# Kernel tuning notes

Hardware: AMD Instinct MI355X
Metric: run time of the kernel (lower is better)

## Reference

```python
import jax, jax.numpy as jnp
import numpy as np

B, T, D = 4, 8192, 512
N_LEVELS = 3
N_HEAD = 4
HEAD_DIM = D // N_HEAD
STRIDES = (8, 4, 4)
SEGS = (T // 8, T // 32, T // 128)  # 1024, 256, 64 segments per level
LN_EPS = 1e-5


def setup_inputs() -> dict:
    key = jax.random.key(0)
    ks = jax.random.split(key, 8)
    h_bytes = jax.random.normal(ks[0], (B, T, D), jnp.float32)
    def strided_boundaries(length, stride):
        b = np.zeros((B, length), np.int32)
        b[:, ::stride] = 1  # segment-start markers; first position always a boundary
        return jnp.asarray(b)
    b0 = strided_boundaries(T, STRIDES[0])
    b1 = strided_boundaries(SEGS[0], STRIDES[1])
    b2 = strided_boundaries(SEGS[1], STRIDES[2])
    s = 0.02
    return dict(
        h_bytes=h_bytes, b0=b0, b1=b1, b2=b2,
        mlp_ln_g=jnp.ones((N_LEVELS, D), jnp.float32),
        mlp_ln_b=jnp.zeros((N_LEVELS, D), jnp.float32),
        mlp_w1=jax.random.normal(ks[1], (N_LEVELS, D, 2 * D), jnp.float32) * s,
        mlp_b1=jnp.zeros((N_LEVELS, 2 * D), jnp.float32),
        mlp_w2=jax.random.normal(ks[2], (N_LEVELS, 2 * D, D), jnp.float32) * s,
        mlp_b2=jnp.zeros((N_LEVELS, D), jnp.float32),
        # 8 linears per cross-level block: bu_q,bu_k,bu_v,bu_out,td_q,td_k,td_v,td_out
        ca_w=jax.random.normal(ks[3], (N_LEVELS - 1, 8, D, D), jnp.float32) * s,
        ca_b=jnp.zeros((N_LEVELS - 1, 8, D), jnp.float32),
        ca_ln_g=jnp.ones((N_LEVELS - 1, 2, D), jnp.float32),  # [.,0]=bu_norm, [.,1]=td_norm
        ca_ln_b=jnp.zeros((N_LEVELS - 1, 2, D), jnp.float32),
    )


def _ln(x, g, b):
    mu = jnp.mean(x, axis=-1, keepdims=True)
    xc = x - mu
    var = jnp.mean(xc * xc, axis=-1, keepdims=True)
    return xc * jax.lax.rsqrt(var + LN_EPS) * g + b


def _mha(xq, xkv, Wq, Wk, Wv, Wo, bq, bk, bv, bo):
    Bq, Sq, _ = xq.shape
    Skv = xkv.shape[1]
    q = (xq @ Wq + bq).reshape(Bq, Sq, N_HEAD, HEAD_DIM)
    k = (xkv @ Wk + bk).reshape(Bq, Skv, N_HEAD, HEAD_DIM)
    v = (xkv @ Wv + bv).reshape(Bq, Skv, N_HEAD, HEAD_DIM)
    scores = jnp.einsum('bqhd,bkhd->bhqk', q, k) * (1.0 / (HEAD_DIM ** 0.5))
    att = jax.nn.softmax(scores, axis=-1)
    out = jnp.einsum('bhqk,bkhd->bqhd', att, v).reshape(Bq, Sq, D)
    return out @ Wo + bo


def _segment_mean_pool(x, seg_ids, n_seg):
    # x: [B, T, D], seg_ids: [B, T] in [0, n_seg)
    sums = jax.vmap(lambda xi, si: jax.ops.segment_sum(xi, si, num_segments=n_seg))(x, seg_ids)
    cnts = jax.vmap(lambda si: jax.ops.segment_sum(jnp.ones(si.shape, jnp.float32), si, num_segments=n_seg))(seg_ids)
    return sums / jnp.maximum(cnts, 1.0)[..., None]


def reference(h_bytes, b0, b1, b2, mlp_ln_g, mlp_ln_b, mlp_w1, mlp_b1, mlp_w2, mlp_b2, ca_w, ca_b, ca_ln_g, ca_ln_b):
    bounds = (b0, b1, b2)
    segs = []
    cur = h_bytes
    for lvl in range(N_LEVELS):
        seg_ids = jnp.cumsum(bounds[lvl], axis=1) - 1  # boundary marks segment start
        pooled = _segment_mean_pool(cur, seg_ids, SEGS[lvl])
        h = _ln(pooled, mlp_ln_g[lvl], mlp_ln_b[lvl])
        h = jax.nn.gelu(h @ mlp_w1[lvl] + mlp_b1[lvl], approximate=False)
        pooled = pooled + (h @ mlp_w2[lvl] + mlp_b2[lvl])
        segs.append(pooled)
        cur = pooled
    # top-down cross-level refinement
    for i in range(N_LEVELS - 2, -1, -1):
        fine, coarse = segs[i], segs[i + 1]
        fn = _ln(fine, ca_ln_g[i, 0], ca_ln_b[i, 0])
        fu = fine + _mha(fn, coarse, ca_w[i, 0], ca_w[i, 1], ca_w[i, 2], ca_w[i, 3],
                         ca_b[i, 0], ca_b[i, 1], ca_b[i, 2], ca_b[i, 3])
        cn = _ln(coarse, ca_ln_g[i, 1], ca_ln_b[i, 1])
        cu = coarse + _mha(cn, fu, ca_w[i, 4], ca_w[i, 5], ca_w[i, 6], ca_w[i, 7],
                           ca_b[i, 4], ca_b[i, 5], ca_b[i, 6], ca_b[i, 7])
        segs[i], segs[i + 1] = fu, cu
    return tuple(segs)
```

## Files before the change

kernel.cpp:

```cpp
#include <hip/hip_runtime.h>
#include <hip/hip_bf16.h>
#include <math.h>

typedef __attribute__((ext_vector_type(8))) short bf16x8;
typedef __attribute__((ext_vector_type(4))) float f32x4;
typedef unsigned short u16;

__device__ __forceinline__ u16 f2b(float f) {
  unsigned u = __float_as_uint(f);
  u = u + 0x7fffu + ((u >> 16) & 1u);
  return (u16)(u >> 16);
}
__device__ __forceinline__ float gelu_exact(float x) {
  return 0.5f * x * (1.0f + erff(x * 0.70710678118654752f));
}

__global__ __launch_bounds__(1024) void scan_all_k(
    const int* __restrict__ b0, const int* __restrict__ b1,
    const int* __restrict__ b2, int* __restrict__ starts) {
  __shared__ int sums[1024];
  int lvl = blockIdx.y, row = blockIdx.x;
  const int* bp = (lvl == 0) ? b0 : (lvl == 1) ? b1 : b2;
  int n = (lvl == 0) ? 8192 : (lvl == 1) ? 1024 : 256;
  int nseg = (lvl == 0) ? 1024 : (lvl == 1) ? 256 : 64;
  int* sp = starts + ((lvl == 0) ? 0 : (lvl == 1) ? 4096 : 5120);
  const int* br = bp + (size_t)row * n;
  int chunk = (n + 1023) / 1024;
  int t0 = threadIdx.x * chunk;
  int t1 = t0 + chunk; if (t1 > n) t1 = n;
  if (t0 > n) t0 = n;
  int s = 0;
  for (int t = t0; t < t1; ++t) s += br[t];
  sums[threadIdx.x] = s;
  __syncthreads();
  for (int off = 1; off < 1024; off <<= 1) {
    int v = (threadIdx.x >= off) ? sums[threadIdx.x - off] : 0;
    __syncthreads();
    sums[threadIdx.x] += v;
    __syncthreads();
  }
  int run = sums[threadIdx.x] - s;
  for (int t = t0; t < t1; ++t) {
    if (br[t]) { sp[(size_t)row * nseg + run] = t; ++run; }
  }
}

__global__ __launch_bounds__(256) void wtrans_all_k(
    const float* __restrict__ w1, const float* __restrict__ w2,
    const float* __restrict__ ca, u16* __restrict__ w1t,
    u16* __restrict__ w2t, u16* __restrict__ cat) {
  __shared__ float tile[32][33];
  int z = blockIdx.x;
  const float* W; u16* Wt; int K, M, m0, k0;
  if (z < 1536) {
    int mat = z >> 9, tl = z & 511;
    W = w1 + (size_t)mat * 524288; Wt = w1t + (size_t)mat * 524288;
    K = 512; M = 1024; m0 = (tl & 31) * 32; k0 = (tl >> 5) * 32;
  } else if (z < 3072) {
    z -= 1536; int mat = z >> 9, tl = z & 511;
    W = w2 + (size_t)mat * 524288; Wt = w2t + (size_t)mat * 524288;
    K = 1024; M = 512; m0 = (tl & 15) * 32; k0 = (tl >> 4) * 32;
  } else {
    z -= 3072; int mat = z >> 8, tl = z & 255;
    W = ca + (size_t)mat * 262144; Wt = cat + (size_t)mat * 262144;
    K = 512; M = 512; m0 = (tl & 15) * 32; k0 = (tl >> 4) * 32;
  }
  int x = threadIdx.x & 31, y = threadIdx.x >> 5;
  #pragma unroll
  for (int i = 0; i < 32; i += 8)
    tile[y + i][x] = W[(size_t)(k0 + y + i) * M + m0 + x];
  __syncthreads();
  #pragma unroll
  for (int i = 0; i < 32; i += 8)
    Wt[(size_t)(m0 + y + i) * K + k0 + x] = f2b(tile[x][y + i]);
}

__global__ __launch_bounds__(256) void pool_ln_k(
    const float* __restrict__ x, const int* __restrict__ starts,
    float* __restrict__ pooled, const float* __restrict__ g,
    const float* __restrict__ bt, u16* __restrict__ lnout,
    int Tin, int nseg) {
  int wv = threadIdx.x >> 6, lane = threadIdx.x & 63;
  int s = blockIdx.x * 4 + wv, b = blockIdx.y;
  int st = starts[(size_t)b * nseg + s];
  int en = (s + 1 < nseg) ? starts[(size_t)b * nseg + s + 1] : Tin;
  const float* xb = x + ((size_t)b * Tin) * 512;
  int d = lane * 8;
  float a[8] = {0.f,0.f,0.f,0.f,0.f,0.f,0.f,0.f};
  for (int t = st; t < en; ++t) {
    const float* row = xb + (size_t)t * 512 + d;
    float4 v0 = *(const float4*)row;
    float4 v1 = *(const float4*)(row + 4);
    a[0]+=v0.x; a[1]+=v0.y; a[2]+=v0.z; a[3]+=v0.w;
    a[4]+=v1.x; a[5]+=v1.y; a[6]+=v1.z; a[7]+=v1.w;
  }
  int cnt = en - st; if (cnt < 1) cnt = 1;
  float ic = 1.0f / (float)cnt;
  #pragma unroll
  for (int i = 0; i < 8; ++i) a[i] *= ic;
  int tok = b * nseg + s;
  float* pr = pooled + (size_t)tok * 512 + d;
  *(float4*)pr = make_float4(a[0], a[1], a[2], a[3]);
  *(float4*)(pr + 4) = make_float4(a[4], a[5], a[6], a[7]);
  float sm = a[0]+a[1]+a[2]+a[3]+a[4]+a[5]+a[6]+a[7];
  #pragma unroll
  for (int off = 32; off; off >>= 1) sm += __shfl_xor(sm, off, 64);
  float mean = sm * (1.0f / 512.0f);
  float ss = 0.f;
  #pragma unroll
  for (int i = 0; i < 8; ++i) { a[i] -= mean; ss += a[i]*a[i]; }
  #pragma unroll
  for (int off = 32; off; off >>= 1) ss += __shfl_xor(ss, off, 64);
  float inv = rsqrtf(ss * (1.0f / 512.0f) + 1e-5f);
  float4 g0 = *(const float4*)(g + d), g1 = *(const float4*)(g + d + 4);
  float4 b0 = *(const float4*)(bt + d), b1 = *(const float4*)(bt + d + 4);
  float gg[8] = {g0.x,g0.y,g0.z,g0.w,g1.x,g1.y,g1.z,g1.w};
  float bb[8] = {b0.x,b0.y,b0.z,b0.w,b1.x,b1.y,b1.z,b1.w};
  union { u16 u[8]; uint4 v; } pk;
  #pragma unroll
  for (int i = 0; i < 8; ++i) pk.u[i] = f2b(a[i] * inv * gg[i] + bb[i]);
  *(uint4*)(lnout + (size_t)tok * 512 + d) = pk.v;
}

__global__ __launch_bounds__(256) void ln_kernel(
    const float* __restrict__ x, const float* __restrict__ g,
    const float* __restrict__ bt, u16* __restrict__ y, int ntok) {
  int wave = threadIdx.x >> 6, lane = threadIdx.x & 63;
  int tok = blockIdx.x * 4 + wave;
  if (tok >= ntok) return;
  const float* xr = x + (size_t)tok * 512;
  int d = lane * 8;
  float4 v0 = *(const float4*)(xr + d);
  float4 v1 = *(const float4*)(xr + d + 4);
  float s = v0.x + v0.y + v0.z + v0.w + v1.x + v1.y + v1.z + v1.w;
  #pragma unroll
  for (int off = 32; off; off >>= 1) s += __shfl_xor(s, off, 64);
  float mean = s * (1.0f / 512.0f);
  float a[8] = {v0.x-mean, v0.y-mean, v0.z-mean, v0.w-mean,
                v1.x-mean, v1.y-mean, v1.z-mean, v1.w-mean};
  float ss = 0.f;
  #pragma unroll
  for (int i = 0; i < 8; ++i) ss += a[i]*a[i];
  #pragma unroll
  for (int off = 32; off; off >>= 1) ss += __shfl_xor(ss, off, 64);
  float inv = rsqrtf(ss * (1.0f / 512.0f) + 1e-5f);
  float4 g0 = *(const float4*)(g + d), g1 = *(const float4*)(g + d + 4);
  float4 b0 = *(const float4*)(bt + d), b1 = *(const float4*)(bt + d + 4);
  float gg[8] = {g0.x,g0.y,g0.z,g0.w,g1.x,g1.y,g1.z,g1.w};
  float bb[8] = {b0.x,b0.y,b0.z,b0.w,b1.x,b1.y,b1.z,b1.w};
  union { u16 u[8]; uint4 v; } pk;
  #pragma unroll
  for (int i = 0; i < 8; ++i) pk.u[i] = f2b(a[i] * inv * gg[i] + bb[i]);
  *(uint4*)(y + (size_t)tok * 512 + d) = pk.v;
}

__global__ __launch_bounds__(256) void vtrans_kernel(
    const u16* __restrict__ vsrc, int lds_, u16* __restrict__ vT, int Skv) {
  __shared__ u16 tile[32][33];
  int kv0 = blockIdx.x * 32, d0 = blockIdx.y * 32;
  int z = blockIdx.z, b = z >> 2, h = z & 3;
  const u16* src = vsrc + ((size_t)b * Skv) * lds_ + h * 128;
  u16* dst = vT + (size_t)z * 128 * Skv;
  int x = threadIdx.x & 31, y = threadIdx.x >> 5;
  #pragma unroll
  for (int i = 0; i < 32; i += 8)
    tile[y + i][x] = src[(size_t)(kv0 + y + i) * lds_ + d0 + x];
  __syncthreads();
  #pragma unroll
  for (int i = 0; i < 32; i += 8)
    dst[(size_t)(d0 + y + i) * Skv + kv0 + x] = tile[x][y + i];
}

__device__ __forceinline__ void mfma_core(
    const u16* __restrict__ A, int lda, const u16* __restrict__ Wt, int ldw,
    int K, u16* AsB, u16* WsB, f32x4 acc[2][2]) {
  int t = threadIdx.x;
  int lane = t & 63, wave = t >> 6;
  int wr = (wave >> 1) * 32, wc = (wave & 1) * 32;
  int lrow = t >> 3;
  int lseg = t & 7;
  int swz = (lseg * 16) ^ ((lrow & 7) << 4);
  const u16* Ap0 = A + (size_t)lrow * lda + lseg * 8;
  const u16* Ap1 = Ap0 + (size_t)32 * lda;
  const u16* Wp0 = Wt + (size_t)lrow * ldw + lseg * 8;
  const u16* Wp1 = Wp0 + (size_t)32 * ldw;
  uint4 a0 = *(const uint4*)(Ap0);
  uint4 a1 = *(const uint4*)(Ap1);
  uint4 w0 = *(const uint4*)(Wp0);
  uint4 w1 = *(const uint4*)(Wp1);
  for (int k0 = 0; k0 < K; k0 += 64) {
    __syncthreads();
    *(uint4*)((char*)AsB + lrow * 128 + swz) = a0;
    *(uint4*)((char*)AsB + (lrow + 32) * 128 + swz) = a1;
    *(uint4*)((char*)WsB + lrow * 128 + swz) = w0;
    *(uint4*)((char*)WsB + (lrow + 32) * 128 + swz) = w1;
    __syncthreads();
    if (k0 + 64 < K) {
      a0 = *(const uint4*)(Ap0 + k0 + 64);
      a1 = *(const uint4*)(Ap1 + k0 + 64);
      w0 = *(const uint4*)(Wp0 + k0 + 64);
      w1 = *(const uint4*)(Wp1 + k0 + 64);
    }
    #pragma unroll
    for (int ks = 0; ks < 2; ++ks) {
      bf16x8 af[2], bfr[2];
      #pragma unroll
      for (int mi = 0; mi < 2; ++mi) {
        int row = wr + mi * 16 + (lane & 15);
        int cb = (ks * 64 + ((lane >> 4) << 4)) ^ ((row & 7) << 4);
        af[mi] = *(const bf16x8*)((const char*)AsB + row * 128 + cb);
      }
      #pragma unroll
      for (int ni = 0; ni < 2; ++ni) {
        int row = wc + ni * 16 + (lane & 15);
        int cb = (ks * 64 + ((lane >> 4) << 4)) ^ ((row & 7) << 4);
        bfr[ni] = *(const bf16x8*)((const char*)WsB + row * 128 + cb);
      }
      #pragma unroll
      for (int mi = 0; mi < 2; ++mi)
        #pragma unroll
        for (int ni = 0; ni < 2; ++ni)
          acc[mi][ni] = __builtin_amdgcn_mfma_f32_16x16x32_bf16(
              af[mi], bfr[ni], acc[mi][ni], 0, 0, 0);
    }
  }
}

__global__ __launch_bounds__(256) void gemm_k(
    const u16* __restrict__ A, int lda, const u16* __restrict__ Wt, int ldw,
    int K, const float* __restrict__ bias, float* __restrict__ Cf,
    u16* __restrict__ Cb, int ldc, int flags) {
  __shared__ u16 As[4096], Ws[4096];
  int n0 = blockIdx.y * 64, m0 = blockIdx.x * 64;
  f32x4 acc[2][2];
  #pragma unroll
  for (int i = 0; i < 2; ++i)
    #pragma unroll
    for (int j = 0; j < 2; ++j) acc[i][j] = (f32x4){0.f, 0.f, 0.f, 0.f};
  mfma_core(A + (size_t)n0 * lda, lda, Wt + (size_t)m0 * ldw, ldw, K, As, Ws, acc);
  int lane = threadIdx.x & 63, wave = threadIdx.x >> 6;
  int wr = (wave >> 1) * 32, wc = (wave & 1) * 32;
  #pragma unroll
  for (int mi = 0; mi < 2; ++mi) {
    #pragma unroll
    for (int ni = 0; ni < 2; ++ni) {
      int col = m0 + wc + ni * 16 + (lane & 15);
      float bv = bias[col];
      #pragma unroll
      for (int j = 0; j < 4; ++j) {
        int row = n0 + wr + mi * 16 + ((lane >> 4) << 2) + j;
        float v = acc[mi][ni][j] + bv;
        if (flags & 1) v = gelu_exact(v);
        size_t idx = (size_t)row * ldc + col;
        if (flags & 2) v += Cf[idx];
        if (flags & 4) Cf[idx] = v;
        if (flags & 8) Cb[idx] = f2b(v);
      }
    }
  }
}

__global__ __launch_bounds__(256) void fattn_k(
    const u16* __restrict__ Q, int ldq, const u16* __restrict__ KV, int ldkv,
    const u16* __restrict__ vT, u16* __restrict__ O, int ldo,
    int Sq, int Skv) {
  __shared__ u16 Ps[4][16 * 64];
  __shared__ float Ob[3][8][16][16];
  __shared__ float Ls[3][16];
  int z = blockIdx.y, b = z >> 2, h = z & 3;
  int t = threadIdx.x, lane = t & 63, w = t >> 6;
  int g = lane >> 4, ql = lane & 15;
  int q0 = blockIdx.x * 16;
  const float scale = 0.08838834764831845f;
  bf16x8 qf[4];
  {
    const u16* qp = Q + ((size_t)(b * Sq + q0 + ql)) * ldq + h * 128 + g * 8;
    #pragma unroll
    for (int ks = 0; ks < 4; ++ks) qf[ks] = *(const bf16x8*)(qp + 32 * ks);
  }
  f32x4 o[8];
  #pragma unroll
  for (int i = 0; i < 8; ++i) o[i] = (f32x4){0.f, 0.f, 0.f, 0.f};
  float lsum = 0.f;
  int ntiles = Skv >> 6;
  const u16* kbaseA = KV + ((size_t)b * Skv + ql) * ldkv + h * 128 + g * 8;
  const u16* vbase = vT + (size_t)z * 128 * Skv;
  for (int tt = w; tt < ntiles; tt += 4) {
    int kv0 = tt * 64;
    float rs = 0.f;
    #pragma unroll
    for (int kvt = 0; kvt < 4; ++kvt) {
      const u16* kp = kbaseA + (size_t)(kv0 + kvt * 16) * ldkv;
      f32x4 acc = (f32x4){0.f, 0.f, 0.f, 0.f};
      #pragma unroll
      for (int ks = 0; ks < 4; ++ks) {
        bf16x8 kf = *(const bf16x8*)(kp + 32 * ks);
        acc = __builtin_amdgcn_mfma_f32_16x16x32_bf16(kf, qf[ks], acc, 0, 0, 0);
      }
      float e0 = __expf(acc[0] * scale), e1 = __expf(acc[1] * scale);
      float e2 = __expf(acc[2] * scale), e3 = __expf(acc[3] * scale);
      rs += e0 + e1 + e2 + e3;
      unsigned lo = (unsigned)f2b(e0) | ((unsigned)f2b(e1) << 16);
      unsigned hi = (unsigned)f2b(e2) | ((unsigned)f2b(e3) << 16);
      int slot = (2 * kvt + (g >> 1)) ^ (ql & 7);
      *(uint2*)((char*)Ps[w] + ql * 128 + slot * 16 + 8 * (g & 1)) =
          make_uint2(lo, hi);
    }
    rs += __shfl_xor(rs, 16, 64);
    rs += __shfl_xor(rs, 32, 64);
    lsum += rs;
    #pragma unroll
    for (int kh = 0; kh < 2; ++kh) {
      int slot = (4 * kh + g) ^ (ql & 7);
      bf16x8 pa = *(const bf16x8*)((const char*)Ps[w] + ql * 128 + slot * 16);
      #pragma unroll
      for (int dt = 0; dt < 8; ++dt) {
        bf16x8 vf = *(const bf16x8*)(vbase + (size_t)(dt * 16 + ql) * Skv +
                                     kv0 + kh * 32 + g * 8);
        o[dt] = __builtin_amdgcn_mfma_f32_16x16x32_bf16(pa, vf, o[dt], 0, 0, 0);
      }
    }
  }
  if (w) {
    #pragma unroll
    for (int dt = 0; dt < 8; ++dt)
      #pragma unroll
      for (int j = 0; j < 4; ++j)
        Ob[w - 1][dt][4 * g + j][ql] = o[dt][j];
    if (g == 0) Ls[w - 1][ql] = lsum;
  }
  __syncthreads();
  if (w == 0) {
    float lt = lsum + Ls[0][ql] + Ls[1][ql] + Ls[2][ql];
    float linv[4];
    #pragma unroll
    for (int r = 0; r < 4; ++r) linv[r] = 1.0f / __shfl(lt, 4 * g + r, 64);
    u16* ob = O + ((size_t)(b * Sq + q0)) * ldo + h * 128;
    #pragma unroll
    for (int dt = 0; dt < 8; ++dt)
      #pragma unroll
      for (int r = 0; r < 4; ++r) {
        float v = o[dt][r] + Ob[0][dt][4 * g + r][ql] +
                  Ob[1][dt][4 * g + r][ql] + Ob[2][dt][4 * g + r][ql];
        ob[(size_t)(4 * g + r) * ldo + dt * 16 + ql] = f2b(v * linv[r]);
      }
  }
}

extern "C" void kernel_launch(void* const* d_in, const int* in_sizes, int n_in,
                              void* d_out, int out_size, void* d_ws, size_t ws_size,
                              hipStream_t stream) {
  (void)in_sizes; (void)n_in; (void)out_size; (void)ws_size;
  const float* h_bytes  = (const float*)d_in[0];
  const int*   b0       = (const int*)d_in[1];
  const int*   b1       = (const int*)d_in[2];
  const int*   b2       = (const int*)d_in[3];
  const float* mlp_ln_g = (const float*)d_in[4];
  const float* mlp_ln_b = (const float*)d_in[5];
  const float* mlp_w1   = (const float*)d_in[6];
  const float* mlp_b1   = (const float*)d_in[7];
  const float* mlp_w2   = (const float*)d_in[8];
  const float* mlp_b2   = (const float*)d_in[9];
  const float* ca_w     = (const float*)d_in[10];
  const float* ca_b     = (const float*)d_in[11];
  const float* ca_ln_g  = (const float*)d_in[12];
  const float* ca_ln_b  = (const float*)d_in[13];

  float* out0 = (float*)d_out;
  float* out1 = out0 + 4 * 1024 * 512;
  float* out2 = out1 + 4 * 256 * 512;

  char* wsb = (char*)d_ws;
  const size_t MB = 1048576;
  u16* w1t   = (u16*)(wsb + 0 * MB);
  u16* w2t   = (u16*)(wsb + 3 * MB);
  u16* cat   = (u16*)(wsb + 6 * MB);
  u16* m0b   = (u16*)(wsb + 14 * MB);
  u16* m1b   = (u16*)(wsb + 18 * MB);
  u16* m2b   = (u16*)(wsb + 19 * MB);
  u16* lnbuf = (u16*)(wsb + 20 * MB);
  u16* hbuf  = (u16*)(wsb + 24 * MB);
  u16* qb    = (u16*)(wsb + 32 * MB);
  u16* kvbuf = (u16*)(wsb + 36 * MB);
  u16* vT    = (u16*)(wsb + 44 * MB);
  u16* abuf  = (u16*)(wsb + 48 * MB);
  int* starts  = (int*)(wsb + 52 * MB);
  int* starts0 = starts;
  int* starts1 = starts + 4096;
  int* starts2 = starts + 5120;

  wtrans_all_k<<<7168, 256, 0, stream>>>(mlp_w1, mlp_w2, ca_w, w1t, w2t, cat);
  scan_all_k<<<dim3(4, 3), 1024, 0, stream>>>(b0, b1, b2, starts);

  auto mlp = [&](float* X, u16* mir, int Ntok, int lvl) {
    gemm_k<<<dim3(16, Ntok / 64), 256, 0, stream>>>(
        lnbuf, 512, w1t + (size_t)lvl * 524288, 512, 512,
        mlp_b1 + lvl * 1024, nullptr, hbuf, 1024, 1 | 8);
    gemm_k<<<dim3(8, Ntok / 64), 256, 0, stream>>>(
        hbuf, 1024, w2t + (size_t)lvl * 524288, 1024, 1024,
        mlp_b2 + lvl * 512, X, mir, 512, 2 | 4 | 8);
  };
  pool_ln_k<<<dim3(256, 4), 256, 0, stream>>>(h_bytes, starts0, out0,
      mlp_ln_g, mlp_ln_b, lnbuf, 8192, 1024);
  mlp(out0, m0b, 4096, 0);
  pool_ln_k<<<dim3(64, 4), 256, 0, stream>>>(out0, starts1, out1,
      mlp_ln_g + 512, mlp_ln_b + 512, lnbuf, 1024, 256);
  mlp(out1, m1b, 1024, 1);
  pool_ln_k<<<dim3(16, 4), 256, 0, stream>>>(out1, starts2, out2,
      mlp_ln_g + 1024, mlp_ln_b + 1024, lnbuf, 256, 64);
  mlp(out2, m2b, 256, 2);

  auto cross = [&](int i, float* F, u16* mf, float* Cc, u16* mc, int nf, int nc) {
    u16* cw = cat + (size_t)i * 8 * 262144;
    const float* bb = ca_b + (size_t)i * 8 * 512;
    const float* lg = ca_ln_g + (size_t)i * 2 * 512;
    const float* lb = ca_ln_b + (size_t)i * 2 * 512;
    int Nf = 4 * nf, Nc = 4 * nc;
    ln_kernel<<<Nf / 4, 256, 0, stream>>>(F, lg, lb, lnbuf, Nf);
    gemm_k<<<dim3(8, Nf / 64), 256, 0, stream>>>(lnbuf, 512, cw, 512, 512,
        bb, nullptr, qb, 512, 8);
    gemm_k<<<dim3(16, Nc / 64), 256, 0, stream>>>(mc, 512, cw + 262144, 512, 512,
        bb + 512, nullptr, kvbuf, 1024, 8);
    vtrans_kernel<<<dim3(nc / 32, 4, 16), 256, 0, stream>>>(kvbuf + 512, 1024, vT, nc);
    fattn_k<<<dim3(nf / 16, 16), 256, 0, stream>>>(qb, 512, kvbuf, 1024, vT,
        abuf, 512, nf, nc);
    gemm_k<<<dim3(8, Nf / 64), 256, 0, stream>>>(abuf, 512, cw + 3 * 262144, 512, 512,
        bb + 3 * 512, F, mf, 512, 2 | 4 | 8);
    ln_kernel<<<Nc / 4, 256, 0, stream>>>(Cc, lg + 512, lb + 512, lnbuf, Nc);
    gemm_k<<<dim3(8, Nc / 64), 256, 0, stream>>>(lnbuf, 512, cw + 4 * 262144, 512, 512,
        bb + 4 * 512, nullptr, qb, 512, 8);
    gemm_k<<<dim3(16, Nf / 64), 256, 0, stream>>>(mf, 512, cw + 5 * 262144, 512, 512,
        bb + 5 * 512, nullptr, kvbuf, 1024, 8);
    vtrans_kernel<<<dim3(nf / 32, 4, 16), 256, 0, stream>>>(kvbuf + 512, 1024, vT, nf);
    fattn_k<<<dim3(nc / 16, 16), 256, 0, stream>>>(qb, 512, kvbuf, 1024, vT,
        abuf, 512, nc, nf);
    gemm_k<<<dim3(8, Nc / 64), 256, 0, stream>>>(abuf, 512, cw + 7 * 262144, 512, 512,
        bb + 7 * 512, Cc, mc, 512, 2 | 4 | 8);
  };
  cross(1, out1, m1b, out2, m2b, 256, 64);
  cross(0, out0, m0b, out1, m1b, 1024, 256);
}
```

Measured before the change: 443.0 us.

## Fuse LN, GEMM and V-transpose into multi-job kernels to cut launches

Merges the weight transpose and boundary scan into one kernel and replaces the separate LayerNorm, GEMM and V-transpose launches with a single fused kernel that dispatches LN blocks and up to two GEMM jobs by block index. The K/V projection writes V already transposed through a shared-memory tile, which removes the vtrans pass. Independent stages, such as the next LayerNorm alongside the output projection and the Q and KV GEMMs, now run in one grid. Bf16 mirror writes that are never read are dropped. This reduces launch count and serialization, at the cost of more branching and a larger shared-memory footprint per block.

```diff
diff --git a/kernel.cpp b/kernel.cpp
--- a/kernel.cpp
+++ b/kernel.cpp
@@ -15,42 +15,47 @@
   return 0.5f * x * (1.0f + erff(x * 0.70710678118654752f));
 }
 
-__global__ __launch_bounds__(1024) void scan_all_k(
+struct GemmJob {
+  const u16* A; const u16* Wt; const float* bias;
+  float* Cf; u16* Cb; u16* vT;
+  int lda, ldw, K, ldc, flags, bx, nblk, Skv;
+};
+struct LnJob { const float* x; const float* g; const float* b; u16* y; int ntok, nblk; };
+
+__global__ __launch_bounds__(256) void wtrans_scan_k(
+    const float* __restrict__ w1, const float* __restrict__ w2,
+    const float* __restrict__ ca, u16* __restrict__ w1t,
+    u16* __restrict__ w2t, u16* __restrict__ cat,
     const int* __restrict__ b0, const int* __restrict__ b1,
     const int* __restrict__ b2, int* __restrict__ starts) {
-  __shared__ int sums[1024];
-  int lvl = blockIdx.y, row = blockIdx.x;
-  const int* bp = (lvl == 0) ? b0 : (lvl == 1) ? b1 : b2;
-  int n = (lvl == 0) ? 8192 : (lvl == 1) ? 1024 : 256;
-  int nseg = (lvl == 0) ? 1024 : (lvl == 1) ? 256 : 64;
-  int* sp = starts + ((lvl == 0) ? 0 : (lvl == 1) ? 4096 : 5120);
-  const int* br = bp + (size_t)row * n;
-  int chunk = (n + 1023) / 1024;
-  int t0 = threadIdx.x * chunk;
-  int t1 = t0 + chunk; if (t1 > n) t1 = n;
-  if (t0 > n) t0 = n;
-  int s = 0;
-  for (int t = t0; t < t1; ++t) s += br[t];
-  sums[threadIdx.x] = s;
-  __syncthreads();
-  for (int off = 1; off < 1024; off <<= 1) {
-    int v = (threadIdx.x >= off) ? sums[threadIdx.x - off] : 0;
+  __shared__ char smbuf[32 * 33 * 4];
+  int z = blockIdx.x;
+  if (z >= 7168) {
+    int* sums = (int*)smbuf;
+    int j = z - 7168, lvl = j >> 2, row = j & 3;
+    const int* bp = (lvl == 0) ? b0 : (lvl == 1) ? b1 : b2;
+    int n = (lvl == 0) ? 8192 : (lvl == 1) ? 1024 : 256;
+    int nseg = (lvl == 0) ? 1024 : (lvl == 1) ? 256 : 64;
+    int* sp = starts + ((lvl == 0) ? 0 : (lvl == 1) ? 4096 : 5120);
+    const int* br = bp + (size_t)row * n;
+    int chunk = n >> 8;
+    int t0 = threadIdx.x * chunk, t1 = t0 + chunk;
+    int s = 0;
+    for (int t = t0; t < t1; ++t) s += br[t];
+    sums[threadIdx.x] = s;
     __syncthreads();
-    sums[threadIdx.x] += v;
-    __syncthreads();
-  }
-  int run = sums[threadIdx.x] - s;
-  for (int t = t0; t < t1; ++t) {
-    if (br[t]) { sp[(size_t)row * nseg + run] = t; ++run; }
-  }
-}
-
-__global__ __launch_bounds__(256) void wtrans_all_k(
-    const float* __restrict__ w1, const float* __restrict__ w2,
-    const float* __restrict__ ca, u16* __restrict__ w1t,
-    u16* __restrict__ w2t, u16* __restrict__ cat) {
-  __shared__ float tile[32][33];
-  int z = blockIdx.x;
+    for (int off = 1; off < 256; off <<= 1) {
+      int v = (threadIdx.x >= off) ? sums[threadIdx.x - off] : 0;
+      __syncthreads();
+      sums[threadIdx.x] += v;
+      __syncthreads();
+    }
+    int run = sums[threadIdx.x] - s;
+    for (int t = t0; t < t1; ++t)
+      if (br[t]) { sp[(size_t)row * nseg + run] = t; ++run; }
+    return;
+  }
+  float (*tile)[33] = (float(*)[33])smbuf;
   const float* W; u16* Wt; int K, M, m0, k0;
   if (z < 1536) {
     int mat = z >> 9, tl = z & 511;
@@ -120,55 +125,6 @@
   #pragma unroll
   for (int i = 0; i < 8; ++i) pk.u[i] = f2b(a[i] * inv * gg[i] + bb[i]);
   *(uint4*)(lnout + (size_t)tok * 512 + d) = pk.v;
-}
-
-__global__ __launch_bounds__(256) void ln_kernel(
-    const float* __restrict__ x, const float* __restrict__ g,
-    const float* __restrict__ bt, u16* __restrict__ y, int ntok) {
-  int wave = threadIdx.x >> 6, lane = threadIdx.x & 63;
-  int tok = blockIdx.x * 4 + wave;
-  if (tok >= ntok) return;
-  const float* xr = x + (size_t)tok * 512;
-  int d = lane * 8;
-  float4 v0 = *(const float4*)(xr + d);
-  float4 v1 = *(const float4*)(xr + d + 4);
-  float s = v0.x + v0.y + v0.z + v0.w + v1.x + v1.y + v1.z + v1.w;
-  #pragma unroll
-  for (int off = 32; off; off >>= 1) s += __shfl_xor(s, off, 64);
-  float mean = s * (1.0f / 512.0f);
-  float a[8] = {v0.x-mean, v0.y-mean, v0.z-mean, v0.w-mean,
-                v1.x-mean, v1.y-mean, v1.z-mean, v1.w-mean};
-  float ss = 0.f;
-  #pragma unroll
-  for (int i = 0; i < 8; ++i) ss += a[i]*a[i];
-  #pragma unroll
-  for (int off = 32; off; off >>= 1) ss += __shfl_xor(ss, off, 64);
-  float inv = rsqrtf(ss * (1.0f / 512.0f) + 1e-5f);
-  float4 g0 = *(const float4*)(g + d), g1 = *(const float4*)(g + d + 4);
-  float4 b0 = *(const float4*)(bt + d), b1 = *(const float4*)(bt + d + 4);
-  float gg[8] = {g0.x,g0.y,g0.z,g0.w,g1.x,g1.y,g1.z,g1.w};
-  float bb[8] = {b0.x,b0.y,b0.z,b0.w,b1.x,b1.y,b1.z,b1.w};
-  union { u16 u[8]; uint4 v; } pk;
-  #pragma unroll
-  for (int i = 0; i < 8; ++i) pk.u[i] = f2b(a[i] * inv * gg[i] + bb[i]);
-  *(uint4*)(y + (size_t)tok * 512 + d) = pk.v;
-}
-
-__global__ __launch_bounds__(256) void vtrans_kernel(
-    const u16* __restrict__ vsrc, int lds_, u16* __restrict__ vT, int Skv) {
-  __shared__ u16 tile[32][33];
-  int kv0 = blockIdx.x * 32, d0 = blockIdx.y * 32;
-  int z = blockIdx.z, b = z >> 2, h = z & 3;
-  const u16* src = vsrc + ((size_t)b * Skv) * lds_ + h * 128;
-  u16* dst = vT + (size_t)z * 128 * Skv;
-  int x = threadIdx.x & 31, y = threadIdx.x >> 5;
-  #pragma unroll
-  for (int i = 0; i < 32; i += 8)
-    tile[y + i][x] = src[(size_t)(kv0 + y + i) * lds_ + d0 + x];
-  __syncthreads();
-  #pragma unroll
-  for (int i = 0; i < 32; i += 8)
-    dst[(size_t)(d0 + y + i) * Skv + kv0 + x] = tile[x][y + i];
 }
 
 __device__ __forceinline__ void mfma_core(
@@ -226,37 +182,108 @@
   }
 }
 
-__global__ __launch_bounds__(256) void gemm_k(
-    const u16* __restrict__ A, int lda, const u16* __restrict__ Wt, int ldw,
-    int K, const float* __restrict__ bias, float* __restrict__ Cf,
-    u16* __restrict__ Cb, int ldc, int flags) {
-  __shared__ u16 As[4096], Ws[4096];
-  int n0 = blockIdx.y * 64, m0 = blockIdx.x * 64;
+__device__ __forceinline__ void gemm_body(const GemmJob& J, int mx, int my,
+                                          char* smem) {
+  u16* As = (u16*)smem;
+  u16* Ws = As + 4096;
+  int n0 = my * 64, m0 = mx * 64;
   f32x4 acc[2][2];
   #pragma unroll
   for (int i = 0; i < 2; ++i)
     #pragma unroll
     for (int j = 0; j < 2; ++j) acc[i][j] = (f32x4){0.f, 0.f, 0.f, 0.f};
-  mfma_core(A + (size_t)n0 * lda, lda, Wt + (size_t)m0 * ldw, ldw, K, As, Ws, acc);
+  mfma_core(J.A + (size_t)n0 * J.lda, J.lda, J.Wt + (size_t)m0 * J.ldw, J.ldw,
+            J.K, As, Ws, acc);
   int lane = threadIdx.x & 63, wave = threadIdx.x >> 6;
   int wr = (wave >> 1) * 32, wc = (wave & 1) * 32;
+  if ((J.flags & 16) && m0 >= 512) {
+    __syncthreads();
+    u16* tile = (u16*)smem;
+    #pragma unroll
+    for (int mi = 0; mi < 2; ++mi)
+      #pragma unroll
+      for (int ni = 0; ni < 2; ++ni) {
+        int tc = wc + ni * 16 + (lane & 15);
+        float bv = J.bias[m0 + tc];
+        #pragma unroll
+        for (int j = 0; j < 4; ++j) {
+          int tr = wr + mi * 16 + ((lane >> 4) << 2) + j;
+          tile[tr * 72 + tc] = f2b(acc[mi][ni][j] + bv);
+        }
+      }
+    __syncthreads();
+    int h = (m0 - 512) >> 7, d0i = (m0 - 512) & 127;
+    int b = n0 / J.Skv, tok0 = n0 % J.Skv;
+    int z = b * 4 + h;
+    int d = threadIdx.x >> 2, tkb = (threadIdx.x & 3) * 16;
+    u16* dst = J.vT + ((size_t)z * 128 + d0i + d) * J.Skv + tok0 + tkb;
+    union { u16 u[16]; uint4 v[2]; } pk;
+    #pragma unroll
+    for (int t2 = 0; t2 < 16; ++t2) pk.u[t2] = tile[(tkb + t2) * 72 + d];
+    *(uint4*)dst = pk.v[0];
+    *(uint4*)(dst + 8) = pk.v[1];
+    return;
+  }
   #pragma unroll
   for (int mi = 0; mi < 2; ++mi) {
     #pragma unroll
     for (int ni = 0; ni < 2; ++ni) {
       int col = m0 + wc + ni * 16 + (lane & 15);
-      float bv = bias[col];
+      float bv = J.bias[col];
       #pragma unroll
       for (int j = 0; j < 4; ++j) {
         int row = n0 + wr + mi * 16 + ((lane >> 4) << 2) + j;
         float v = acc[mi][ni][j] + bv;
-        if (flags & 1) v = gelu_exact(v);
-        size_t idx = (size_t)row * ldc + col;
-        if (flags & 2) v += Cf[idx];
-        if (flags & 4) Cf[idx] = v;
-        if (flags & 8) Cb[idx] = f2b(v);
+        if (J.flags & 1) v = gelu_exact(v);
+        size_t idx = (size_t)row * J.ldc + col;
+        if (J.flags & 2) v += J.Cf[idx];
+        if (J.flags & 4) J.Cf[idx] = v;
+        if (J.flags & 8) J.Cb[idx] = f2b(v);
       }
     }
+  }
+}
+
+__device__ __forceinline__ void ln_body(const LnJob& L, int bid) {
+  int wave = threadIdx.x >> 6, lane = threadIdx.x & 63;
+  int tok = bid * 4 + wave;
+  if (tok >= L.ntok) return;
+  const float* xr = L.x + (size_t)tok * 512;
+  int d = lane * 8;
+  float4 v0 = *(const float4*)(xr + d);
+  float4 v1 = *(const float4*)(xr + d + 4);
+  float s = v0.x + v0.y + v0.z + v0.w + v1.x + v1.y + v1.z + v1.w;
+  #pragma unroll
+  for (int off = 32; off; off >>= 1) s += __shfl_xor(s, off, 64);
+  float mean = s * (1.0f / 512.0f);
+  float a[8] = {v0.x-mean, v0.y-mean, v0.z-mean, v0.w-mean,
+                v1.x-mean, v1.y-mean, v1.z-mean, v1.w-mean};
+  float ss = 0.f;
+  #pragma unroll
+  for (int i = 0; i < 8; ++i) ss += a[i]*a[i];
+  #pragma unroll
+  for (int off = 32; off; off >>= 1) ss += __shfl_xor(ss, off, 64);
+  float inv = rsqrtf(ss * (1.0f / 512.0f) + 1e-5f);
+  float4 g0 = *(const float4*)(L.g + d), g1 = *(const float4*)(L.g + d + 4);
+  float4 b0 = *(const float4*)(L.b + d), b1 = *(const float4*)(L.b + d + 4);
+  float gg[8] = {g0.x,g0.y,g0.z,g0.w,g1.x,g1.y,g1.z,g1.w};
+  float bb[8] = {b0.x,b0.y,b0.z,b0.w,b1.x,b1.y,b1.z,b1.w};
+  union { u16 u[8]; uint4 v; } pk;
+  #pragma unroll
+  for (int i = 0; i < 8; ++i) pk.u[i] = f2b(a[i] * inv * gg[i] + bb[i]);
+  *(uint4*)(L.y + (size_t)tok * 512 + d) = pk.v;
+}
+
+__global__ __launch_bounds__(256) void fused_k(LnJob L, GemmJob A, GemmJob B) {
+  __shared__ char smem[16384];
+  int bid = blockIdx.x;
+  if (bid < L.nblk) { ln_body(L, bid); return; }
+  bid -= L.nblk;
+  if (bid < A.nblk) {
+    gemm_body(A, bid % A.bx, bid / A.bx, smem);
+  } else {
+    bid -= A.nblk;
+    gemm_body(B, bid % B.bx, bid / B.bx, smem);
   }
 }
 
@@ -381,7 +408,7 @@
   u16* lnbuf = (u16*)(wsb + 20 * MB);
   u16* hbuf  = (u16*)(wsb + 24 * MB);
   u16* qb    = (u16*)(wsb + 32 * MB);
-  u16* kvbuf = (u16*)(wsb + 36 * MB);
+  u16* kbuf  = (u16*)(wsb + 36 * MB);
   u16* vT    = (u16*)(wsb + 44 * MB);
   u16* abuf  = (u16*)(wsb + 48 * MB);
   int* starts  = (int*)(wsb + 52 * MB);
@@ -389,54 +416,90 @@
   int* starts1 = starts + 4096;
   int* starts2 = starts + 5120;
 
-  wtrans_all_k<<<7168, 256, 0, stream>>>(mlp_w1, mlp_w2, ca_w, w1t, w2t, cat);
-  scan_all_k<<<dim3(4, 3), 1024, 0, stream>>>(b0, b1, b2, starts);
-
-  auto mlp = [&](float* X, u16* mir, int Ntok, int lvl) {
-    gemm_k<<<dim3(16, Ntok / 64), 256, 0, stream>>>(
-        lnbuf, 512, w1t + (size_t)lvl * 524288, 512, 512,
-        mlp_b1 + lvl * 1024, nullptr, hbuf, 1024, 1 | 8);
-    gemm_k<<<dim3(8, Ntok / 64), 256, 0, stream>>>(
-        hbuf, 1024, w2t + (size_t)lvl * 524288, 1024, 1024,
-        mlp_b2 + lvl * 512, X, mir, 512, 2 | 4 | 8);
+  auto mkgemm = [](const u16* A, int lda, const u16* Wt, int ldw, int K,
+                   const float* bias, float* Cf, u16* Cb, int ldc, int flags,
+                   int rows, int M, u16* vTp = nullptr, int Skv = 0) {
+    GemmJob j; j.A = A; j.lda = lda; j.Wt = Wt; j.ldw = ldw; j.K = K;
+    j.bias = bias; j.Cf = Cf; j.Cb = Cb; j.ldc = ldc; j.flags = flags;
+    j.bx = M / 64; j.nblk = (M / 64) * (rows / 64); j.vT = vTp; j.Skv = Skv;
+    return j;
   };
+  auto mkln = [](const float* x, const float* g, const float* b, u16* y,
+                 int ntok) {
+    LnJob l; l.x = x; l.g = g; l.b = b; l.y = y; l.ntok = ntok;
+    l.nblk = ntok / 4; return l;
+  };
+  GemmJob gz = {}; gz.nblk = 0; gz.bx = 1;
+  LnJob lz = {}; lz.nblk = 0;
+  auto launch = [&](LnJob L, GemmJob A, GemmJob B) {
+    fused_k<<<L.nblk + A.nblk + B.nblk, 256, 0, stream>>>(L, A, B);
+  };
+
+  wtrans_scan_k<<<7180, 256, 0, stream>>>(mlp_w1, mlp_w2, ca_w, w1t, w2t, cat,
+                                          b0, b1, b2, starts);
+
   pool_ln_k<<<dim3(256, 4), 256, 0, stream>>>(h_bytes, starts0, out0,
       mlp_ln_g, mlp_ln_b, lnbuf, 8192, 1024);
-  mlp(out0, m0b, 4096, 0);
+  launch(lz, mkgemm(lnbuf, 512, w1t, 512, 512, mlp_b1, nullptr, hbuf, 1024,
+                    1 | 8, 4096, 1024), gz);
+  launch(lz, mkgemm(hbuf, 1024, w2t, 1024, 1024, mlp_b2, out0, nullptr, 512,
+                    2 | 4, 4096, 512), gz);
   pool_ln_k<<<dim3(64, 4), 256, 0, stream>>>(out0, starts1, out1,
       mlp_ln_g + 512, mlp_ln_b + 512, lnbuf, 1024, 256);
-  mlp(out1, m1b, 1024, 1);
+  launch(lz, mkgemm(lnbuf, 512, w1t + 524288, 512, 512, mlp_b1 + 1024,
+                    nullptr, hbuf, 1024, 1 | 8, 1024, 1024), gz);
+  launch(lz, mkgemm(hbuf, 1024, w2t + 524288, 1024, 1024, mlp_b2 + 512, out1,
+                    nullptr, 512, 2 | 4, 1024, 512), gz);
   pool_ln_k<<<dim3(16, 4), 256, 0, stream>>>(out1, starts2, out2,
       mlp_ln_g + 1024, mlp_ln_b + 1024, lnbuf, 256, 64);
-  mlp(out2, m2b, 256, 2);
-
-  auto cross = [&](int i, float* F, u16* mf, float* Cc, u16* mc, int nf, int nc) {
-    u16* cw = cat + (size_t)i * 8 * 262144;
-    const float* bb = ca_b + (size_t)i * 8 * 512;
-    const float* lg = ca_ln_g + (size_t)i * 2 * 512;
-    const float* lb = ca_ln_b + (size_t)i * 2 * 512;
-    int Nf = 4 * nf, Nc = 4 * nc;
-    ln_kernel<<<Nf / 4, 256, 0, stream>>>(F, lg, lb, lnbuf, Nf);
-    gemm_k<<<dim3(8, Nf / 64), 256, 0, stream>>>(lnbuf, 512, cw, 512, 512,
-        bb, nullptr, qb, 512, 8);
-    gemm_k<<<dim3(16, Nc / 64), 256, 0, stream>>>(mc, 512, cw + 262144, 512, 512,
-        bb + 512, nullptr, kvbuf, 1024, 8);
-    vtrans_kernel<<<dim3(nc / 32, 4, 16), 256, 0, stream>>>(kvbuf + 512, 1024, vT, nc);
-    fattn_k<<<dim3(nf / 16, 16), 256, 0, stream>>>(qb, 512, kvbuf, 1024, vT,
-        abuf, 512, nf, nc);
-    gemm_k<<<dim3(8, Nf / 64), 256, 0, stream>>>(abuf, 512, cw + 3 * 262144, 512, 512,
-        bb + 3 * 512, F, mf, 512, 2 | 4 | 8);
-    ln_kernel<<<Nc / 4, 256, 0, stream>>>(Cc, lg + 512, lb + 512, lnbuf, Nc);
-    gemm_k<<<dim3(8, Nc / 64), 256, 0, stream>>>(lnbuf, 512, cw + 4 * 262144, 512, 512,
-        bb + 4 * 512, nullptr, qb, 512, 8);
-    gemm_k<<<dim3(16, Nf / 64), 256, 0, stream>>>(mf, 512, cw + 5 * 262144, 512, 512,
-        bb + 5 * 512, nullptr, kvbuf, 1024, 8);
-    vtrans_kernel<<<dim3(nf / 32, 4, 16), 256, 0, stream>>>(kvbuf + 512, 1024, vT, nf);
-    fattn_k<<<dim3(nc / 16, 16), 256, 0, stream>>>(qb, 512, kvbuf, 1024, vT,
-        abuf, 512, nc, nf);
-    gemm_k<<<dim3(8, Nc / 64), 256, 0, stream>>>(abuf, 512, cw + 7 * 262144, 512, 512,
-        bb + 7 * 512, Cc, mc, 512, 2 | 4 | 8);
-  };
-  cross(1, out1, m1b, out2, m2b, 256, 64);
-  cross(0, out0, m0b, out1, m1b, 1024, 256);
-}
+  launch(lz, mkgemm(lnbuf, 512, w1t + 2 * 524288, 512, 512, mlp_b1 + 2048,
+                    nullptr, hbuf, 1024, 1 | 8, 256, 1024), gz);
+  launch(lz, mkgemm(hbuf, 1024, w2t + 2 * 524288, 1024, 1024, mlp_b2 + 1024,
+                    out2, m2b, 512, 2 | 4 | 8, 256, 512), gz);
+
+  const size_t WS = 262144;
+  {
+    u16* cw = cat + 8 * WS;
+    const float* bb = ca_b + 8 * 512;
+    launch(mkln(out1, ca_ln_g + 1024, ca_ln_b + 1024, lnbuf, 1024),
+           mkgemm(m2b, 512, cw + WS, 512, 512, bb + 512, nullptr, kbuf, 512,
+                  8 | 16, 256, 1024, vT, 64), gz);
+    launch(lz, mkgemm(lnbuf, 512, cw, 512, 512, bb, nullptr, qb, 512, 8,
+                      1024, 512), gz);
+    fattn_k<<<dim3(16, 16), 256, 0, stream>>>(qb, 512, kbuf, 512, vT, abuf,
+                                              512, 256, 64);
+    launch(mkln(out2, ca_ln_g + 1536, ca_ln_b + 1536, lnbuf, 256),
+           mkgemm(abuf, 512, cw + 3 * WS, 512, 512, bb + 3 * 512, out1, m1b,
+                  512, 2 | 4 | 8, 1024, 512), gz);
+    launch(lz, mkgemm(lnbuf, 512, cw + 4 * WS, 512, 512, bb + 4 * 512,
+                      nullptr, qb, 512, 8, 256, 512),
+           mkgemm(m1b, 512, cw + 5 * WS, 512, 512, bb + 5 * 512, nullptr,
+                  kbuf, 512, 8 | 16, 1024, 1024, vT, 256));
+    fattn_k<<<dim3(4, 16), 256, 0, stream>>>(qb, 512, kbuf, 512, vT, abuf,
+                                             512, 64, 256);
+    launch(mkln(out0, ca_ln_g, ca_ln_b, lnbuf, 4096),
+           mkgemm(abuf, 512, cw + 7 * WS, 512, 512, bb + 7 * 512, out2,
+                  nullptr, 512, 2 | 4, 256, 512), gz);
+  }
+  {
+    u16* cw = cat;
+    const float* bb = ca_b;
+    launch(lz, mkgemm(lnbuf, 512, cw, 512, 512, bb, nullptr, qb, 512, 8,
+                      4096, 512),
+           mkgemm(m1b, 512, cw + WS, 512, 512, bb + 512, nullptr, kbuf, 512,
+                  8 | 16, 1024, 1024, vT, 256));
+    fattn_k<<<dim3(64, 16), 256, 0, stream>>>(qb, 512, kbuf, 512, vT, abuf,
+                                              512, 1024, 256);
+    launch(mkln(out1, ca_ln_g + 512, ca_ln_b + 512, lnbuf, 1024),
+           mkgemm(abuf, 512, cw + 3 * WS, 512, 512, bb + 3 * 512, out0, m0b,
+                  512, 2 | 4 | 8, 4096, 512), gz);
+    launch(lz, mkgemm(lnbuf, 512, cw + 4 * WS, 512, 512, bb + 4 * 512,
+                      nullptr, qb, 512, 8, 1024, 512),
+           mkgemm(m0b, 512, cw + 5 * WS, 512, 512, bb + 5 * 512, nullptr,
+                  kbuf, 512, 8 | 16, 4096, 1024, vT, 1024));
+    fattn_k<<<dim3(16, 16), 256, 0, stream>>>(qb, 512, kbuf, 512, vT, abuf,
+                                              512, 256, 1024);
+    launch(lz, mkgemm(abuf, 512, cw + 7 * WS, 512, 512, bb + 7 * 512, out1,
+                      nullptr, 512, 2 | 4, 1024, 512), gz);
+  }
+}
```

New measurement: 417.5 us. 5.7% less time.
